# Kernel optimization log

Hardware: AMD Instinct MI355X
Metric: run time of the kernel (lower is better)

## Reference

```python
import jax, jax.numpy as jnp
import numpy as np
from jax import lax

EPS = 1e-5

def _bn(x):
    # BatchNorm1d, training-mode batch stats, affine at init (gamma=1, beta=0)
    return (x - x.mean(0)) / jnp.sqrt(x.var(0) + EPS)

def _nonlinear(x, W1, W2):
    h = jax.nn.relu(_bn(x @ W1.T))
    return jax.nn.relu(_bn(h @ W2.T))

def _conv_bn_lrelu(x, w):
    # x: [E, C, L], w: [O, C, 3], padding=1; BN over (batch, length)
    y = lax.conv_general_dilated(x, w, (1,), [(1, 1)], dimension_numbers=('NCH', 'OIH', 'NCH'))
    m = y.mean((0, 2), keepdims=True)
    v = y.var((0, 2), keepdims=True)
    y = (y - m) / jnp.sqrt(v + EPS)
    return jnp.where(y >= 0, y, 0.01 * y)  # LeakyReLU(negative_slope=0.01)

def _curve_encoder(x, c1, c2, c3, fc):
    y = _conv_bn_lrelu(x, c1)
    y = _conv_bn_lrelu(y, c2)
    y = _conv_bn_lrelu(y, c3)
    y = y.mean(-1)            # AdaptiveAvgPool1d(1)
    return _bn(y @ fc.T)      # _fc: Linear(bias=False) + BN, no activation

def _forward(attn_bias, angle, centroid_distance, edge_data, edge_type,
             edge_length, edge_convexity, node_feat,
             sd_emb, virt, angle_W1, angle_W2, cent_W1, cent_W2,
             etype_W1, etype_W2, elen_W1, elen_W2, econv_W1, econv_W2,
             curv_c1, curv_c2, curv_c3, curv_fc, edis_w,
             ec_Wp, ec_W1, ec_W2,
             shortest_distance, edge_path, edge_padding_mask, src, dst):
    B, N, _ = shortest_distance.shape
    H = sd_emb.shape[1]
    D = edge_path.shape[-1]           # multi_hop_max_dist
    n_edge = edge_padding_mask.shape[1]

    bias = jnp.broadcast_to(attn_bias[:, None], (B, H, N + 1, N + 1))

    # shortest-distance / angle / centroid biases, all [B, H, N, N]
    sdb = sd_emb[shortest_distance].transpose(0, 3, 1, 2)
    ang = _nonlinear(angle.reshape(-1, 1), angle_W1, angle_W2).reshape(B, N, N, H).transpose(0, 3, 1, 2)
    cen = _nonlinear(centroid_distance.reshape(-1, 1), cent_W1, cent_W2).reshape(B, N, N, H).transpose(0, 3, 1, 2)

    # --- multi_hop branch ---
    ef = (_curve_encoder(edge_data.transpose(0, 2, 1), curv_c1, curv_c2, curv_c3, curv_fc)
          + _nonlinear(edge_type, etype_W1, etype_W2)
          + _nonlinear(edge_length[:, None], elen_W1, elen_W2)
          + _nonlinear(edge_convexity, econv_W1, econv_W2))     # [E, H]
    # EdgeConv (UV-Net style node_cat): proj(n[src]) + proj(n[dst]) + efeat -> MLP -> BN -> ReLU
    proj = node_feat @ ec_Wp.T
    agg = proj[src] + proj[dst] + ef
    h = jax.nn.relu(_bn(agg @ ec_W1.T)) @ ec_W2.T
    ef2 = jax.nn.relu(_bn(h))                                   # [E, H]

    # edge_padding_mask is all-False, so edge_feature[edge_pos] = ef2 is a plain
    # row-major reshape; slot n_edge stays zero (padding target of edge_path)
    edge_feature = jnp.zeros((B, n_edge + 1, H), dtype=edge_data.dtype)
    edge_feature = edge_feature.at[:, :n_edge].set(ef2.reshape(B, n_edge, H))

    sd_ = jnp.where(shortest_distance == 0, 1, shortest_distance)
    sd_ = jnp.where(sd_ > 1, sd_ - 1, sd_)
    sd_ = jnp.clip(sd_, 0, D)

    ep = edge_path.reshape(B, N * N * D)
    eb = jnp.take_along_axis(edge_feature, ep[:, :, None], axis=1).reshape(B, N, N, D, H)
    Wd = edis_w.reshape(-1, H, H)[:D]                           # [D, H, H]
    eb = jnp.einsum('bijdh,dhk->bijk', eb, Wd)                  # per-hop bmm fused with hop-sum
    eb = eb / (sd_.astype(eb.dtype)[..., None] + 1e-6)
    eb = jnp.nan_to_num(eb)
    ebias = eb.transpose(0, 3, 1, 2)                            # [B, H, N, N]

    bias = bias.at[:, :, 1:, 1:].add(sdb + ang + cen + ebias)
    t = virt.reshape(1, H, 1)
    bias = bias.at[:, :, 1:, 0].add(t)
    bias = bias.at[:, :, 0, :].add(t)
    return bias + attn_bias[:, None]


def setup_inputs() -> dict:
    key = jax.random.key(0)
    ks = iter(jax.random.split(key, 48))
    B, N, H, D = 4, 256, 16, 5
    n_edge, n_pts = 1024, 20
    dim_node, num_distance, num_edge_dis = 256, 512, 128
    E = B * n_edge
    tot_nodes = B * N
    rn = lambda *s: jax.random.normal(next(ks), s, jnp.float32)
    return {
        'attn_bias': rn(B, N + 1, N + 1),
        'shortest_distance': jax.random.randint(next(ks), (B, N, N), 0, num_distance),
        'angle': rn(B, N, N),
        'centroid_distance': rn(B, N, N),
        'edge_path': jax.random.randint(next(ks), (B, N, N, D), 0, n_edge + 1),
        'edge_data': rn(E, n_pts, 12),
        'edge_type': rn(E, 11),
        'edge_length': rn(E),
        'edge_convexity': rn(E, 3),
        'edge_padding_mask': jnp.zeros((B, n_edge), dtype=bool),
        'src': jax.random.randint(next(ks), (E,), 0, tot_nodes),
        'dst': jax.random.randint(next(ks), (E,), 0, tot_nodes),
        'node_feat': rn(tot_nodes, dim_node),
        'sd_emb': (rn(num_distance, H) * 0.02).at[0].set(0.0),  # padding_idx=0
        'virt': rn(1, H) * 0.02,
        'angle_W1': rn(H, 1) * 0.1, 'angle_W2': rn(H, H) * 0.1,
        'cent_W1': rn(H, 1) * 0.1, 'cent_W2': rn(H, H) * 0.1,
        'etype_W1': rn(H, 11) * 0.1, 'etype_W2': rn(H, H) * 0.1,
        'elen_W1': rn(H, 1) * 0.1, 'elen_W2': rn(H, H) * 0.1,
        'econv_W1': rn(H, 3) * 0.1, 'econv_W2': rn(H, H) * 0.1,
        'curv_c1': rn(64, 12, 3) * 0.1, 'curv_c2': rn(128, 64, 3) * 0.05,
        'curv_c3': rn(256, 128, 3) * 0.05, 'curv_fc': rn(H, 256) * 0.05,
        'edis_w': rn(num_edge_dis * H * H, 1) * 0.02,
        'ec_Wp': rn(H, dim_node) * 0.02, 'ec_W1': rn(64, H) * 0.02, 'ec_W2': rn(H, 64) * 0.02,
    }


def reference(attn_bias, shortest_distance, angle, centroid_distance, edge_path,
              edge_data, edge_type, edge_length, edge_convexity, edge_padding_mask,
              src, dst, node_feat, sd_emb, virt, angle_W1, angle_W2, cent_W1, cent_W2,
              etype_W1, etype_W2, elen_W1, elen_W2, econv_W1, econv_W2,
              curv_c1, curv_c2, curv_c3, curv_fc, edis_w, ec_Wp, ec_W1, ec_W2):
    return _forward(attn_bias, angle, centroid_distance, edge_data, edge_type,
                    edge_length, edge_convexity, node_feat,
                    sd_emb, virt, angle_W1, angle_W2, cent_W1, cent_W2,
                    etype_W1, etype_W2, elen_W1, elen_W2, econv_W1, econv_W2,
                    curv_c1, curv_c2, curv_c3, curv_fc, edis_w,
                    ec_Wp, ec_W1, ec_W2,
                    shortest_distance, edge_path, edge_padding_mask, src, dst)
```

## Files before the change

### kernel.cpp

```cpp
#include <hip/hip_runtime.h>

#define EPSB 1e-5f
#define B_ 4
#define N_ 256
#define H_ 16
#define D_ 5
#define E_ 4096
#define M_PAIR (B_*N_*N_)

typedef __attribute__((ext_vector_type(8))) short short8;
typedef __attribute__((ext_vector_type(4))) float f32x4;

enum {
  SO_ANGX = 0,
  SO_CENX = 2,
  SO_MOMA = 16,
  SO_MOMC = 24,
  SO_C1   = 96,  SO_C1Q   = 160,
  SO_C2   = 224, SO_C2Q   = 352,
  SO_C3   = 480, SO_C3Q   = 736,
  SO_FC   = 992, SO_FCQ   = 1008,
  SO_ET1  = 1024, SO_ET1Q = 1040,
  SO_ET2  = 1056, SO_ET2Q = 1072,
  SO_EL1  = 1088, SO_EL1Q = 1104,
  SO_EL2  = 1120, SO_EL2Q = 1136,
  SO_EV1  = 1152, SO_EV1Q = 1168,
  SO_EV2  = 1184, SO_EV2Q = 1200,
  SO_G1   = 1216, SO_G1Q  = 1280,
  SO_G2   = 1344, SO_G2Q  = 1360,
  STATS_FLOATS = 2048
};

static constexpr size_t F_Y13  = 2048;
static constexpr size_t F_Y2   = F_Y13 + 10485760;
static constexpr size_t F_POOL = F_Y2 + 5242880;
static constexpr size_t F_FCB  = F_POOL + 1048576;
static constexpr size_t F_EF   = F_FCB + 65536;
static constexpr size_t F_PROJ = F_EF + 65536;
static constexpr size_t F_Z1EC = F_PROJ + 16384;
static constexpr size_t F_Z2T  = F_Z1EC + 262144;
static constexpr size_t F_G    = F_Z2T + 196608;
static constexpr size_t F_WT2  = F_G + 328000;
static constexpr size_t F_WT3  = F_WT2 + 12288;

__device__ __forceinline__ float waveSum(float v){
  #pragma unroll
  for(int o=32;o;o>>=1) v += __shfl_down(v,o);
  return v;
}

__device__ __forceinline__ ushort f2bf(float f){
  uint u = __float_as_uint(f);
  uint r = (u + 0x7FFF + ((u>>16)&1)) >> 16;
  return (ushort)r;
}
__device__ __forceinline__ float bf2f(ushort u){
  return __uint_as_float(((uint)u)<<16);
}

__device__ __forceinline__ void red32_atomic(float* ws, int so, int soq, float* s, float* q){
  __shared__ float red[4][32];
  int tid=threadIdx.x, lane=tid&63, wid=tid>>6;
  #pragma unroll
  for(int k=0;k<16;k++){
    float rs=waveSum(s[k]), rq=waveSum(q[k]);
    if(lane==0){ red[wid][k]=rs; red[wid][16+k]=rq; }
  }
  __syncthreads();
  if(tid<32){
    float t=red[0][tid]+red[1][tid]+red[2][tid]+red[3][tid];
    atomicAdd(&ws[tid<16 ? so+tid : soq+(tid-16)], t);
  }
}

__global__ __launch_bounds__(256) void k_conv1(const float* __restrict__ ed,
    const float* __restrict__ w, float* __restrict__ ws){
  __shared__ float wsh[64*37];
  __shared__ float xs[8*12*20];
  __shared__ float reds[256], redq[256];
  int tid=threadIdx.x;
  for(int i=tid;i<2304;i+=256){ int o=i/36, r=i%36; wsh[o*37+r]=w[i]; }
  int e0=blockIdx.x*8;
  for(int i=tid;i<1920;i+=256){
    int e=i/240, r=i%240, l=r/12, c=r%12;
    xs[(e*12+c)*20+l]=ed[(size_t)(e0+e)*240+r];
  }
  __syncthreads();
  int o=tid&63, eg=tid>>6;
  ushort* y1=(ushort*)(ws+F_Y13);
  float ssum=0, ssq=0;
  for(int ee=0;ee<2;ee++){
    int e=eg*2+ee;
    float acc[20];
    #pragma unroll
    for(int l=0;l<20;l++) acc[l]=0;
    for(int c=0;c<12;c++){
      float w0=wsh[o*37+c*3], w1=wsh[o*37+c*3+1], w2=wsh[o*37+c*3+2];
      const float* xr=xs+(e*12+c)*20;
      #pragma unroll
      for(int l=0;l<20;l++){
        acc[l]=fmaf(w1,xr[l],acc[l]);
        if(l>0)  acc[l]=fmaf(w0,xr[l-1],acc[l]);
        if(l<19) acc[l]=fmaf(w2,xr[l+1],acc[l]);
      }
    }
    size_t base=((size_t)(e0+e)*20)*64;
    #pragma unroll
    for(int l=0;l<20;l++){
      y1[base+(size_t)l*64+o]=f2bf(acc[l]);
      ssum+=acc[l]; ssq+=acc[l]*acc[l];
    }
  }
  reds[eg*64+o]=ssum; redq[eg*64+o]=ssq;
  __syncthreads();
  if(tid<64){
    atomicAdd(&ws[SO_C1+tid], reds[tid]+reds[64+tid]+reds[128+tid]+reds[192+tid]);
  } else if(tid<128){
    int oo=tid-64;
    atomicAdd(&ws[SO_C1Q+oo], redq[oo]+redq[64+oo]+redq[128+oo]+redq[192+oo]);
  }
}


__device__ void dev_wprep(int bid, const float* __restrict__ c2w,
    const float* __restrict__ c3w, ushort* __restrict__ wt2, ushort* __restrict__ wt3){
  int t = bid*256 + threadIdx.x;
  if(t < 128*192){
    int idx=t;
    int j=idx&7, lane=(idx>>3)&63, ks=(idx>>9)%6, ct=idx/3072;
    int l16=lane&15, lhi=lane>>4;
    int o=ct*16+l16, tap=ks/2, c=(ks%2)*32+lhi*8+j;
    wt2[idx]=f2bf(c2w[(o*64+c)*3+tap]);
  } else {
    int idx=t-128*192;
    if(idx<256*384){
      int j=idx&7, lane=(idx>>3)&63, ks=(idx>>9)%12, ct=idx/6144;
      int l16=lane&15, lhi=lane>>4;
      int o=ct*16+l16, tap=ks/4, c=(ks%4)*32+lhi*8+j;
      wt3[idx]=f2bf(c3w[(o*128+c)*3+tap]);
    }
  }
}

__device__ void dev_proj(int bid, const float* __restrict__ nf,
    const float* __restrict__ Wp, float* __restrict__ ws, char* pool){
  float* wps=(float*)pool;
  int tid=threadIdx.x;
  for(int i=tid;i<4096;i+=256){ wps[(i>>8)*260+(i&255)]=Wp[i]; }
  __syncthreads();
  int t=bid*256+tid;
  int v=t>>4, h=t&15;
  const float4* row=(const float4*)(nf+(size_t)v*256);
  const float4* wr=(const float4*)(wps+h*260);
  float z=0;
  #pragma unroll 8
  for(int c=0;c<64;c++){
    float4 a=row[c], b=wr[c];
    z+=a.x*b.x+a.y*b.y+a.z*b.z+a.w*b.w;
  }
  ws[F_PROJ+t]=z;
}

__device__ void dev_scalar(int bid, const float* __restrict__ ang,
    const float* __restrict__ cen, float* __restrict__ st){
  int tid = bid*256 + threadIdx.x;
  float sa=0, qa=0, sc=0, qc=0;
  for(int i=tid; i<M_PAIR; i += 256*256){
    float a=ang[i], c=cen[i];
    sa+=a; qa+=a*a; sc+=c; qc+=c*c;
  }
  __shared__ float red[4][4];
  int lane=threadIdx.x&63, wid=threadIdx.x>>6;
  sa=waveSum(sa); qa=waveSum(qa); sc=waveSum(sc); qc=waveSum(qc);
  if(lane==0){ red[wid][0]=sa; red[wid][1]=qa; red[wid][2]=sc; red[wid][3]=qc; }
  __syncthreads();
  if(threadIdx.x<4){
    float t=red[0][threadIdx.x]+red[1][threadIdx.x]+red[2][threadIdx.x]+red[3][threadIdx.x];
    atomicAdd(&st[threadIdx.x], t);
  }
}

template<int DIM>
__device__ void dev_sml1(const float* __restrict__ x,
    const float* __restrict__ W1, float* __restrict__ ws, int so, int soq, int bid){
  __shared__ float w1s[176];
  int tid=threadIdx.x;
  if(tid<16*DIM) w1s[tid]=W1[tid];
  __syncthreads();
  int e=bid*256+tid;
  float xv[DIM];
  #pragma unroll
  for(int j=0;j<DIM;j++) xv[j]=x[(size_t)e*DIM+j];
  float s[16], q[16];
  #pragma unroll
  for(int k=0;k<16;k++){
    float z=0;
    #pragma unroll
    for(int j=0;j<DIM;j++) z+=w1s[k*DIM+j]*xv[j];
    s[k]=z; q[k]=z*z;
  }
  red32_atomic(ws, so, soq, s, q);
}

__global__ __launch_bounds__(256) void k_misc(
    const float* __restrict__ c2w, const float* __restrict__ c3w,
    const float* __restrict__ nf, const float* __restrict__ Wp,
    const float* __restrict__ ang, const float* __restrict__ cen,
    const float* __restrict__ et, const float* __restrict__ el, const float* __restrict__ ev,
    const float* __restrict__ etW1, const float* __restrict__ elW1, const float* __restrict__ evW1,
    float* __restrict__ ws){
  __shared__ char pool[16640];
  int bx=blockIdx.x;
  if(bx<480)       dev_wprep(bx, c2w, c3w, (ushort*)(ws+F_WT2), (ushort*)(ws+F_WT3));
  else if(bx<544)  dev_proj(bx-480, nf, Wp, ws, pool);
  else if(bx<800)  dev_scalar(bx-544, ang, cen, ws);
  else {
    int bid=bx-800;
    int g=bid>>4, b2=bid&15;
    if(g==0)      dev_sml1<11>(et,etW1,ws,SO_ET1,SO_ET1Q,b2);
    else if(g==1) dev_sml1<1> (el,elW1,ws,SO_EL1,SO_EL1Q,b2);
    else          dev_sml1<3> (ev,evW1,ws,SO_EV1,SO_EV1Q,b2);
  }
}


__device__ void dev_mom2(int bid, const float* __restrict__ x, float* __restrict__ st,
    int soX, int mo){
  int tid=threadIdx.x;
  float mu = st[soX]*(1.0f/262144.0f);
  float P=0,N=0,Pq=0,Nq=0;
  for(int i=bid*256+tid; i<M_PAIR; i+=32*256){
    float dx=x[i]-mu;
    if(dx>0){ P+=dx; Pq+=dx*dx; } else { N+=dx; Nq+=dx*dx; }
  }
  __shared__ float red[4][4];
  int lane=tid&63, wid=tid>>6;
  P=waveSum(P); N=waveSum(N); Pq=waveSum(Pq); Nq=waveSum(Nq);
  if(lane==0){ red[wid][0]=P; red[wid][1]=N; red[wid][2]=Pq; red[wid][3]=Nq; }
  __syncthreads();
  if(tid<4){
    float t=red[0][tid]+red[1][tid]+red[2][tid]+red[3][tid];
    atomicAdd(&st[mo+tid], t);
  }
}

template<int DIM>
__device__ void dev_sml2(const float* __restrict__ x,
    const float* __restrict__ W1, const float* __restrict__ W2,
    float* __restrict__ ws, int so1, int so1q, int so2, int so2q,
    float* __restrict__ z2out, int bid){
  __shared__ float w1s[176];
  __shared__ float w2s[256];
  __shared__ float mi[16][2];
  int tid=threadIdx.x;
  if(tid<16*DIM) w1s[tid]=W1[tid];
  w2s[tid]=W2[tid];
  if(tid<16){
    float m=ws[so1+tid]*(1.0f/4096.0f);
    float v=ws[so1q+tid]*(1.0f/4096.0f)-m*m; if(v<0)v=0;
    mi[tid][0]=m; mi[tid][1]=rsqrtf(v+EPSB);
  }
  __syncthreads();
  int e=bid*256+tid;
  float xv[DIM];
  #pragma unroll
  for(int j=0;j<DIM;j++) xv[j]=x[(size_t)e*DIM+j];
  float h1[16];
  #pragma unroll
  for(int h=0;h<16;h++){
    float z=0;
    #pragma unroll
    for(int j=0;j<DIM;j++) z+=w1s[h*DIM+j]*xv[j];
    z=(z-mi[h][0])*mi[h][1];
    h1[h]=z>0?z:0;
  }
  float s[16], q[16];
  #pragma unroll
  for(int k=0;k<16;k++){
    float z=0;
    #pragma unroll
    for(int h=0;h<16;h++) z+=w2s[k*16+h]*h1[h];
    z2out[(size_t)e*16+k]=z;
    s[k]=z; q[k]=z*z;
  }
  red32_atomic(ws, so2, so2q, s, q);
}

__global__ __launch_bounds__(256) void k_stats2(
    const float* __restrict__ ang, const float* __restrict__ cen,
    const float* __restrict__ et, const float* __restrict__ el, const float* __restrict__ ev,
    const float* __restrict__ etW1, const float* __restrict__ etW2,
    const float* __restrict__ elW1, const float* __restrict__ elW2,
    const float* __restrict__ evW1, const float* __restrict__ evW2,
    float* __restrict__ ws){
  int bx=blockIdx.x;
  if(bx<32)       dev_mom2(bx, ang, ws, SO_ANGX, SO_MOMA);
  else if(bx<64)  dev_mom2(bx-32, cen, ws, SO_CENX, SO_MOMC);
  else {
    int bid=bx-64;
    int g=bid>>4, b2=bid&15;
    if(g==0)      dev_sml2<11>(et,etW1,etW2,ws,SO_ET1,SO_ET1Q,SO_ET2,SO_ET2Q,ws+F_Z2T,b2);
    else if(g==1) dev_sml2<1> (el,elW1,elW2,ws,SO_EL1,SO_EL1Q,SO_EL2,SO_EL2Q,ws+F_Z2T+65536,b2);
    else          dev_sml2<3> (ev,evW1,evW2,ws,SO_EV1,SO_EV1Q,SO_EV2,SO_EV2Q,ws+F_Z2T+131072,b2);
  }
}

template<int CIN, int OUT, int EPB, int NSPLIT>
__global__ __launch_bounds__(256) void k_convmf(
    const ushort* __restrict__ yin, const ushort* __restrict__ wt,
    ushort* __restrict__ yout, float* __restrict__ ws,
    int soIn, int soInQ, int soOut, int soOutQ)
{
  constexpr int K = CIN*3;
  constexpr int KSTEPS = K/32;
  constexpr int M = EPB*20;
  constexpr int ROWT = M/16;
  constexpr int WCOLT = OUT/(64*NSPLIT);
  constexpr int ROWS = EPB*22;
  constexpr int RBp = CIN*2 + 16;
  constexpr int RWp = RBp/4;
  __shared__ char xsb[ROWS*RBp];
  __shared__ float mi[CIN][2];
  int tid = threadIdx.x;
  int bx = blockIdx.x;
  int eblk = bx / NSPLIT, split = bx % NSPLIT;
  int lane = tid&63, wid = tid>>6;
  int l16 = lane&15, lhi = lane>>4;
  int colbase = (split*4 + wid) * (OUT/(4*NSPLIT));

  short8 bF[WCOLT][KSTEPS];
  #pragma unroll
  for(int n=0;n<WCOLT;n++){
    const ushort* wp = wt + ((size_t)(colbase/16 + n)*KSTEPS)*512 + (size_t)lane*8;
    #pragma unroll
    for(int ks=0;ks<KSTEPS;ks++) bF[n][ks]=*(const short8*)(wp + (size_t)ks*512);
  }

  for(int c=tid; c<CIN; c+=256){
    float m=ws[soIn+c]*(1.0f/81920.0f);
    float v=ws[soInQ+c]*(1.0f/81920.0f)-m*m; if(v<0)v=0;
    mi[c][0]=m; mi[c][1]=rsqrtf(v+EPSB);
  }
  uint* xs32 = (uint*)xsb;
  for(int i=tid; i<EPB*2*(CIN/2); i+=256){
    int e=i/(CIN), r=i%(CIN); int lp = (r < CIN/2)? 0:21; int cw = r%(CIN/2);
    xs32[(e*22+lp)*RWp+cw]=0;
  }
  __syncthreads();
  int e0 = eblk*EPB;
  const ushort* src = yin + (size_t)e0*20*CIN;
  for(int i=tid; i<EPB*20*(CIN/8); i+=256){
    int c8 = i%(CIN/8); int rl = i/(CIN/8);
    int c = c8*8;
    short8 v = *(const short8*)(src + (size_t)rl*CIN + c);
    uint pk[4];
    #pragma unroll
    for(int jj=0;jj<4;jj++){
      float f0 = bf2f((ushort)v[jj*2]);
      float f1 = bf2f((ushort)v[jj*2+1]);
      f0=(f0-mi[c+jj*2  ][0])*mi[c+jj*2  ][1]; f0= f0>=0?f0:0.01f*f0;
      f1=(f1-mi[c+jj*2+1][0])*mi[c+jj*2+1][1]; f1= f1>=0?f1:0.01f*f1;
      pk[jj] = (uint)f2bf(f0) | ((uint)f2bf(f1)<<16);
    }
    int e = rl/20, l=rl%20;
    int row = e*22 + l + 1;
    *(uint4*)(xsb + (size_t)row*RBp + c*2) = make_uint4(pk[0],pk[1],pk[2],pk[3]);
  }
  __syncthreads();

  f32x4 acc[ROWT][WCOLT];
  #pragma unroll
  for(int m=0;m<ROWT;m++)
    #pragma unroll
    for(int n=0;n<WCOLT;n++) acc[m][n]=(f32x4){0,0,0,0};
  int rowc[ROWT];
  #pragma unroll
  for(int m=0;m<ROWT;m++){ int r=m*16+l16; rowc[m]=(r/20)*22 + (r%20); }

  short8 aF0[ROWT], aF1[ROWT];

#define LOADA(ksv, A) { \
    int t_=(ksv)/(CIN/32); int c0_=((ksv)%(CIN/32))*32 + lhi*8; \
    _Pragma("unroll") \
    for(int m=0;m<ROWT;m++){ \
      int row_=rowc[m]+t_; \
      A[m]=*(const short8*)(xsb + (size_t)row_*RBp + c0_*2); } }

#define MFMAK(A, ksv) { \
    _Pragma("unroll") \
    for(int m=0;m<ROWT;m++) \
      _Pragma("unroll") \
      for(int n=0;n<WCOLT;n++) \
        acc[m][n]=__builtin_amdgcn_mfma_f32_16x16x32_bf16(A[m],bF[n][ksv],acc[m][n],0,0,0); }

  LOADA(0, aF0);
  #pragma unroll
  for(int kp=0; kp<KSTEPS/2; kp++){
    LOADA(kp*2+1, aF1);
    MFMAK(aF0, kp*2);
    if(kp*2+2<KSTEPS) LOADA(kp*2+2, aF0);
    MFMAK(aF1, kp*2+1);
  }
#undef LOADA
#undef MFMAK

  #pragma unroll
  for(int n=0;n<WCOLT;n++){
    float s=0,q=0;
    #pragma unroll
    for(int m=0;m<ROWT;m++)
      #pragma unroll
      for(int j=0;j<4;j++){ float a=acc[m][n][j]; s+=a; q+=a*a; }
    s += __shfl_xor(s,16); s += __shfl_xor(s,32);
    q += __shfl_xor(q,16); q += __shfl_xor(q,32);
    if(lhi==0){
      int o = colbase+n*16+l16;
      atomicAdd(&ws[soOut+o], s);
      atomicAdd(&ws[soOutQ+o], q);
    }
  }
  ushort* dst = yout + (size_t)eblk*M*OUT;
  #pragma unroll
  for(int m=0;m<ROWT;m++)
    #pragma unroll
    for(int j=0;j<4;j++){
      int R = m*16 + lhi*4 + j;
      #pragma unroll
      for(int n=0;n<WCOLT;n++)
        dst[(size_t)R*OUT + colbase + n*16 + l16] = f2bf(acc[m][n][j]);
    }
}

__global__ __launch_bounds__(256) void k_poolfc(const float* __restrict__ fcw, float* __restrict__ ws){
  __shared__ float ps[16][260];
  __shared__ float red[4][32];
  __shared__ float mo[256][2];
  int tid=threadIdx.x;
  {
    float m=ws[SO_C3+tid]*(1.0f/81920.0f);
    float v=ws[SO_C3Q+tid]*(1.0f/81920.0f)-m*m; if(v<0)v=0;
    mo[tid][0]=m; mo[tid][1]=rsqrtf(v+EPSB);
  }
  __syncthreads();
  int e0=blockIdx.x*16;
  const ushort* y3=(const ushort*)(ws+F_Y13);
  float m=mo[tid][0], inv=mo[tid][1];
  for(int el=0;el<16;el++){
    const ushort* row=y3+((size_t)(e0+el)*20)*256+tid;
    float s=0;
    #pragma unroll
    for(int l=0;l<20;l++){
      float x=(bf2f(row[(size_t)l*256])-m)*inv;
      s += x>=0.f? x : 0.01f*x;
    }
    ps[el][tid]=s*(1.0f/20.0f);
  }
  __syncthreads();
  int e=tid>>4, h=tid&15;
  const float* wr=fcw+(size_t)h*256;
  float z=0;
  for(int c=0;c<256;c++) z+=ps[e][c]*wr[c];
  ws[F_FCB+(size_t)(e0+e)*16+h]=z;
  float s=z, q=z*z;
  #pragma unroll
  for(int o=16;o<64;o<<=1){ s+=__shfl_down(s,o); q+=__shfl_down(q,o); }
  int lane=tid&63, wid=tid>>6;
  if(lane<16){ red[wid][lane]=s; red[wid][16+lane]=q; }
  __syncthreads();
  if(tid<32){
    float v=red[0][tid]+red[1][tid]+red[2][tid]+red[3][tid];
    atomicAdd(&ws[tid<16? SO_FC+tid : SO_FCQ+(tid-16)], v);
  }
}

__device__ __constant__ int EF_BASES[4][2] = {
  {SO_ET2,SO_ET2Q},{SO_EL2,SO_EL2Q},{SO_EV2,SO_EV2Q},{SO_FC,SO_FCQ}
};

__global__ __launch_bounds__(256) void k_aggef(const int* __restrict__ src, const int* __restrict__ dst,
    const float* __restrict__ ecW1, float* __restrict__ ws){
  __shared__ float w1s[64*17];
  __shared__ float mi[4][16][2];
  __shared__ float aLDS[32][17];
  __shared__ float zLDS[64][33];
  __shared__ float reds[4][64], redq[4][64];
  int tid=threadIdx.x;
  for(int i=tid;i<1024;i+=256) w1s[(i>>4)*17+(i&15)]=ecW1[i];
  if(tid<64){
    int g=tid>>4, h=tid&15;
    float m=ws[EF_BASES[g][0]+h]*(1.0f/4096.0f);
    float v=ws[EF_BASES[g][1]+h]*(1.0f/4096.0f)-m*m; if(v<0)v=0;
    mi[g][h][0]=m; mi[g][h][1]=rsqrtf(v+EPSB);
  }
  __syncthreads();
  int e0=blockIdx.x*32;
  for(int it=tid; it<32*16; it+=256){
    int el=it>>4, h=it&15;
    int e=e0+el;
    float z=ws[F_FCB+(size_t)e*16+h];
    float a=(z-mi[3][h][0])*mi[3][h][1];
    #pragma unroll
    for(int g=0;g<3;g++){
      float z2=ws[F_Z2T+(size_t)g*65536+(size_t)e*16+h];
      float r=(z2-mi[g][h][0])*mi[g][h][1];
      a+= r>0?r:0;
    }
    int s=src[e], d=dst[e];
    a+=ws[F_PROJ+(size_t)s*16+h]+ws[F_PROJ+(size_t)d*16+h];
    aLDS[el][h]=a;
  }
  __syncthreads();
  int o=tid&63, elq=tid>>6;
  float s=0,q=0;
  #pragma unroll
  for(int j=0;j<8;j++){
    int el=elq*8+j;
    float z=0;
    #pragma unroll
    for(int h=0;h<16;h++) z+=w1s[o*17+h]*aLDS[el][h];
    zLDS[o][el]=z;
    s+=z; q+=z*z;
  }
  reds[elq][o]=s; redq[elq][o]=q;
  __syncthreads();
  for(int idx=tid; idx<2048; idx+=256){
    int oo=idx>>5, el=idx&31;
    ws[F_Z1EC+(size_t)oo*E_+e0+el]=zLDS[oo][el];
  }
  if(tid<64){
    atomicAdd(&ws[SO_G1+tid], reds[0][tid]+reds[1][tid]+reds[2][tid]+reds[3][tid]);
  } else if(tid<128){
    int oo=tid-64;
    atomicAdd(&ws[SO_G1Q+oo], redq[0][oo]+redq[1][oo]+redq[2][oo]+redq[3][oo]);
  }
}

__global__ __launch_bounds__(256) void k_ec2(const float* __restrict__ ecW2, float* __restrict__ ws){
  __shared__ float w2s[1024];
  __shared__ float mi[64][2];
  int tid=threadIdx.x;
  for(int i=tid;i<1024;i+=256) w2s[i]=ecW2[i];
  if(tid<64){
    float m=ws[SO_G1+tid]*(1.0f/4096.0f);
    float v=ws[SO_G1Q+tid]*(1.0f/4096.0f)-m*m; if(v<0)v=0;
    mi[tid][0]=m; mi[tid][1]=rsqrtf(v+EPSB);
  }
  __syncthreads();
  int el=tid&63, kq=tid>>6;
  int e=blockIdx.x*64+el;
  float acc[4]={0,0,0,0};
  #pragma unroll 8
  for(int o=0;o<64;o++){
    float z=ws[F_Z1EC+(size_t)o*E_+e];
    float h=(z-mi[o][0])*mi[o][1];
    h=h>0?h:0;
    #pragma unroll
    for(int j=0;j<4;j++) acc[j]+=w2s[(kq*4+j)*64+o]*h;
  }
  #pragma unroll
  for(int j=0;j<4;j++) ws[F_FCB+(size_t)e*16+kq*4+j]=acc[j];
  #pragma unroll
  for(int j=0;j<4;j++){
    float rs=waveSum(acc[j]);
    float rq=waveSum(acc[j]*acc[j]);
    if(el==0){
      atomicAdd(&ws[SO_G2+kq*4+j], rs);
      atomicAdd(&ws[SO_G2Q+kq*4+j], rq);
    }
  }
}

__global__ __launch_bounds__(256) void k_ef2g(const float* __restrict__ edisw, float* __restrict__ ws){
  __shared__ float wd[1280];
  __shared__ float mi[16][2];
  int tid=threadIdx.x;
  for(int i=tid;i<1280;i+=256) wd[i]=edisw[i];
  if(tid<16){
    float m=ws[SO_G2+tid]*(1.0f/4096.0f);
    float va=ws[SO_G2Q+tid]*(1.0f/4096.0f)-m*m; if(va<0)va=0;
    mi[tid][0]=m; mi[tid][1]=rsqrtf(va+EPSB);
  }
  __syncthreads();
  int t=blockIdx.x*256+tid;
  if(t>=4*1025*5) return;
  int bp=t/5, d=t%5;
  int b=bp/1025, pos=bp%1025;
  float ef[16];
  if(pos<1024){
    int e=b*1024+pos;
    #pragma unroll
    for(int k=0;k<16;k++){
      float z=ws[F_FCB+(size_t)e*16+k];
      float v=(z-mi[k][0])*mi[k][1];
      ef[k]= v>0?v:0;
    }
  } else {
    #pragma unroll
    for(int k=0;k<16;k++) ef[k]=0;
  }
  float* g=ws+F_G+(size_t)bp*80+d*16;
  const float* wdd=wd+d*256;
  #pragma unroll
  for(int k=0;k<16;k++){
    float s=0;
    #pragma unroll
    for(int h=0;h<16;h++) s+=ef[h]*wdd[h*16+k];
    g[k]=s;
  }
}

__global__ __launch_bounds__(256) void k_pair(const float* __restrict__ ab,
    const int* __restrict__ sd, const float* __restrict__ ang, const float* __restrict__ cen,
    const int* __restrict__ ep, const float* __restrict__ sdemb,
    const float* __restrict__ angW1, const float* __restrict__ angW2,
    const float* __restrict__ cenW1, const float* __restrict__ cenW2,
    const float* __restrict__ ws, float* __restrict__ out){
  __shared__ float cpa[16],cma[16],m2a[16],i2a[16];
  __shared__ float cpc[16],cmc[16],m2c[16],i2c[16];
  __shared__ float mv[4];
  int tid=threadIdx.x;
  if(tid==0){
    float s=ws[SO_ANGX], q=ws[SO_ANGX+1];
    float mu=s*(1.0f/262144.0f);
    float v=q*(1.0f/262144.0f)-mu*mu; if(v<0)v=0;
    mv[0]=mu; mv[1]=v;
    s=ws[SO_CENX]; q=ws[SO_CENX+1];
    mu=s*(1.0f/262144.0f);
    v=q*(1.0f/262144.0f)-mu*mu; if(v<0)v=0;
    mv[2]=mu; mv[3]=v;
  }
  __syncthreads();
  if(tid<32){
    int k=tid&15; bool isC = tid>=16;
    const float* W1=isC?cenW1:angW1; const float* W2=isC?cenW2:angW2;
    float var=isC?mv[3]:mv[1];
    float cp=0, cm=0;
    for(int h=0;h<16;h++){
      float w=W1[h];
      float A=w*rsqrtf(var*w*w+EPSB);
      float wk=W2[k*16+h];
      if(A>0) cp+=wk*A; else cm+=wk*A;
    }
    int mo = isC? SO_MOMC : SO_MOMA;
    float P=ws[mo], N=ws[mo+1], Pq=ws[mo+2], Nq=ws[mo+3];
    float mean=(cp*P+cm*N)*(1.0f/262144.0f);
    float e2=(cp*cp*Pq+cm*cm*Nq)*(1.0f/262144.0f);
    float v2=e2-mean*mean; if(v2<0)v2=0;
    float iv=rsqrtf(v2+EPSB);
    if(!isC){ cpa[k]=cp; cma[k]=cm; m2a[k]=mean; i2a[k]=iv; }
    else    { cpc[k]=cp; cmc[k]=cm; m2c[k]=mean; i2c[k]=iv; }
  }
  __syncthreads();
  int t=blockIdx.x*256+tid;
  int b=t>>16, rem=t&65535, i=rem>>8, j=rem&255;
  int sdv=sd[t];
  float xa=ang[t], xc0=cen[t];
  float acc[16];
  const float* se=sdemb+(size_t)sdv*16;
  #pragma unroll
  for(int k=0;k<16;k++) acc[k]=se[k];
  {
    float dx=xa-mv[0];
    bool pos=dx>0.f;
    #pragma unroll
    for(int k=0;k<16;k++){
      float z=dx*(pos?cpa[k]:cma[k]);
      float r=(z-m2a[k])*i2a[k];
      acc[k]+= r>0?r:0;
    }
  }
  {
    float dx=xc0-mv[2];
    bool pos=dx>0.f;
    #pragma unroll
    for(int k=0;k<16;k++){
      float z=dx*(pos?cpc[k]:cmc[k]);
      float r=(z-m2c[k])*i2c[k];
      acc[k]+= r>0?r:0;
    }
  }
  {
    int sdm = sdv==0 ? 1 : sdv;
    if(sdm>1) sdm-=1;
    if(sdm>5) sdm=5;
    float inv=1.0f/((float)sdm+1e-6f);
    float eb[16];
    #pragma unroll
    for(int k=0;k<16;k++) eb[k]=0;
    const float* G=ws+F_G;
    #pragma unroll
    for(int d=0;d<5;d++){
      int idx=ep[(size_t)t*5+d];
      const float4* g=(const float4*)(G+(size_t)(b*1025+idx)*80+d*16);
      float4 g0=g[0], g1=g[1], g2=g[2], g3=g[3];
      eb[0]+=g0.x; eb[1]+=g0.y; eb[2]+=g0.z; eb[3]+=g0.w;
      eb[4]+=g1.x; eb[5]+=g1.y; eb[6]+=g1.z; eb[7]+=g1.w;
      eb[8]+=g2.x; eb[9]+=g2.y; eb[10]+=g2.z; eb[11]+=g2.w;
      eb[12]+=g3.x; eb[13]+=g3.y; eb[14]+=g3.z; eb[15]+=g3.w;
    }
    #pragma unroll
    for(int k=0;k<16;k++) acc[k]+=eb[k]*inv;
  }
  float base2=2.0f*ab[(size_t)b*66049+(size_t)(i+1)*257+(j+1)];
  #pragma unroll
  for(int k=0;k<16;k++)
    out[(((size_t)b*16+k)*257+(i+1))*257+(j+1)]=acc[k]+base2;
}

__global__ __launch_bounds__(256) void k_border(const float* __restrict__ ab,
    const float* __restrict__ virt, float* __restrict__ out){
  int t=blockIdx.x*256+threadIdx.x;
  if(t>=4*16*513) return;
  int idx=t%513, bh=t/513;
  int b=bh>>4, h=bh&15;
  float v=virt[h];
  if(idx<257){
    out[(((size_t)b*16+h)*257)*257+idx]=2.0f*ab[(size_t)b*66049+idx]+v;
  } else {
    int p=idx-256;
    out[(((size_t)b*16+h)*257+p)*257]=2.0f*ab[(size_t)b*66049+(size_t)p*257]+v;
  }
}

extern "C" void kernel_launch(void* const* d_in, const int* in_sizes, int n_in,
                              void* d_out, int out_size, void* d_ws, size_t ws_size,
                              hipStream_t stream) {
  const float* ab    =(const float*)d_in[0];
  const int*   sdist =(const int*)  d_in[1];
  const float* ang   =(const float*)d_in[2];
  const float* cen   =(const float*)d_in[3];
  const int*   ep    =(const int*)  d_in[4];
  const float* edata =(const float*)d_in[5];
  const float* etype =(const float*)d_in[6];
  const float* elen  =(const float*)d_in[7];
  const float* econv =(const float*)d_in[8];
  const int*   src   =(const int*)  d_in[10];
  const int*   dst   =(const int*)  d_in[11];
  const float* nf    =(const float*)d_in[12];
  const float* sdemb =(const float*)d_in[13];
  const float* virt  =(const float*)d_in[14];
  const float* angW1 =(const float*)d_in[15];
  const float* angW2 =(const float*)d_in[16];
  const float* cenW1 =(const float*)d_in[17];
  const float* cenW2 =(const float*)d_in[18];
  const float* etW1  =(const float*)d_in[19];
  const float* etW2  =(const float*)d_in[20];
  const float* elW1  =(const float*)d_in[21];
  const float* elW2  =(const float*)d_in[22];
  const float* evW1  =(const float*)d_in[23];
  const float* evW2  =(const float*)d_in[24];
  const float* c1w   =(const float*)d_in[25];
  const float* c2w   =(const float*)d_in[26];
  const float* c3w   =(const float*)d_in[27];
  const float* fcw   =(const float*)d_in[28];
  const float* edisw =(const float*)d_in[29];
  const float* ecWp  =(const float*)d_in[30];
  const float* ecW1  =(const float*)d_in[31];
  const float* ecW2  =(const float*)d_in[32];
  float* ws=(float*)d_ws;
  float* out=(float*)d_out;

  hipMemsetAsync(d_ws, 0, STATS_FLOATS*sizeof(float), stream);

  k_conv1<<<512,256,0,stream>>>(edata,c1w,ws);
  k_misc<<<848,256,0,stream>>>(c2w,c3w,nf,ecWp,ang,cen,
                               etype,elen,econv,etW1,elW1,evW1,ws);
  k_stats2<<<112,256,0,stream>>>(ang,cen,etype,elen,econv,
                                 etW1,etW2,elW1,elW2,evW1,evW2,ws);

  k_convmf<64,128,4,2><<<2048,256,0,stream>>>((const ushort*)(ws+F_Y13),(const ushort*)(ws+F_WT2),
                                              (ushort*)(ws+F_Y2),ws,SO_C1,SO_C1Q,SO_C2,SO_C2Q);
  k_convmf<128,256,4,2><<<2048,256,0,stream>>>((const ushort*)(ws+F_Y2),(const ushort*)(ws+F_WT3),
                                               (ushort*)(ws+F_Y13),ws,SO_C2,SO_C2Q,SO_C3,SO_C3Q);
  k_poolfc<<<256,256,0,stream>>>(fcw,ws);

  k_aggef<<<128,256,0,stream>>>(src,dst,ecW1,ws);
  k_ec2<<<64,256,0,stream>>>(ecW2,ws);
  k_ef2g<<<81,256,0,stream>>>(edisw,ws);

  k_pair<<<1024,256,0,stream>>>(ab,sdist,ang,cen,ep,sdemb,angW1,angW2,cenW1,cenW2,ws,out);
  k_border<<<129,256,0,stream>>>(ab,virt,out);
}
```

Before: 205.3 us.

## Spread conv BN stat atomics over 32 partial slots and XOR-swizzle LDS tile

```diff
diff --git a/kernel.cpp b/kernel.cpp
--- a/kernel.cpp
+++ b/kernel.cpp
@@ -16,9 +16,6 @@
   SO_CENX = 2,
   SO_MOMA = 16,
   SO_MOMC = 24,
-  SO_C1   = 96,  SO_C1Q   = 160,
-  SO_C2   = 224, SO_C2Q   = 352,
-  SO_C3   = 480, SO_C3Q   = 736,
   SO_FC   = 992, SO_FCQ   = 1008,
   SO_ET1  = 1024, SO_ET1Q = 1040,
   SO_ET2  = 1056, SO_ET2Q = 1072,
@@ -28,10 +25,13 @@
   SO_EV2  = 1184, SO_EV2Q = 1200,
   SO_G1   = 1216, SO_G1Q  = 1280,
   SO_G2   = 1344, SO_G2Q  = 1360,
-  STATS_FLOATS = 2048
+  SP_C1   = 2048,
+  SP_C2   = SP_C1 + 32*512,
+  SP_C3   = SP_C2 + 32*512,
+  PSTATS_END = SP_C3 + 32*512
 };
 
-static constexpr size_t F_Y13  = 2048;
+static constexpr size_t F_Y13  = 51200;
 static constexpr size_t F_Y2   = F_Y13 + 10485760;
 static constexpr size_t F_POOL = F_Y2 + 5242880;
 static constexpr size_t F_FCB  = F_POOL + 1048576;
@@ -113,11 +113,12 @@
   }
   reds[eg*64+o]=ssum; redq[eg*64+o]=ssq;
   __syncthreads();
+  int g=blockIdx.x&31;
   if(tid<64){
-    atomicAdd(&ws[SO_C1+tid], reds[tid]+reds[64+tid]+reds[128+tid]+reds[192+tid]);
+    atomicAdd(&ws[SP_C1+g*512+tid], reds[tid]+reds[64+tid]+reds[128+tid]+reds[192+tid]);
   } else if(tid<128){
     int oo=tid-64;
-    atomicAdd(&ws[SO_C1Q+oo], redq[oo]+redq[64+oo]+redq[128+oo]+redq[192+oo]);
+    atomicAdd(&ws[SP_C1+g*512+256+oo], redq[oo]+redq[64+oo]+redq[128+oo]+redq[192+oo]);
   }
 }
 
@@ -309,7 +310,7 @@
 __global__ __launch_bounds__(256) void k_convmf(
     const ushort* __restrict__ yin, const ushort* __restrict__ wt,
     ushort* __restrict__ yout, float* __restrict__ ws,
-    int soIn, int soInQ, int soOut, int soOutQ)
+    int spIn, int spOut)
 {
   constexpr int K = CIN*3;
   constexpr int KSTEPS = K/32;
@@ -317,9 +318,9 @@
   constexpr int ROWT = M/16;
   constexpr int WCOLT = OUT/(64*NSPLIT);
   constexpr int ROWS = EPB*22;
-  constexpr int RBp = CIN*2 + 16;
-  constexpr int RWp = RBp/4;
-  __shared__ char xsb[ROWS*RBp];
+  constexpr int RB = CIN*2;
+  constexpr uint SWZ = RB/16 - 1;
+  __shared__ ushort xs[ROWS*CIN];
   __shared__ float mi[CIN][2];
   int tid = threadIdx.x;
   int bx = blockIdx.x;
@@ -337,14 +338,17 @@
   }
 
   for(int c=tid; c<CIN; c+=256){
-    float m=ws[soIn+c]*(1.0f/81920.0f);
-    float v=ws[soInQ+c]*(1.0f/81920.0f)-m*m; if(v<0)v=0;
+    float s=0,q=0;
+    #pragma unroll
+    for(int g=0;g<32;g++){ s+=ws[spIn+g*512+c]; q+=ws[spIn+g*512+256+c]; }
+    float m=s*(1.0f/81920.0f);
+    float v=q*(1.0f/81920.0f)-m*m; if(v<0)v=0;
     mi[c][0]=m; mi[c][1]=rsqrtf(v+EPSB);
   }
-  uint* xs32 = (uint*)xsb;
+  uint* xs32 = (uint*)xs;
   for(int i=tid; i<EPB*2*(CIN/2); i+=256){
     int e=i/(CIN), r=i%(CIN); int lp = (r < CIN/2)? 0:21; int cw = r%(CIN/2);
-    xs32[(e*22+lp)*RWp+cw]=0;
+    xs32[(e*22+lp)*(CIN/2)+cw]=0;
   }
   __syncthreads();
   int e0 = eblk*EPB;
@@ -364,7 +368,8 @@
     }
     int e = rl/20, l=rl%20;
     int row = e*22 + l + 1;
-    *(uint4*)(xsb + (size_t)row*RBp + c*2) = make_uint4(pk[0],pk[1],pk[2],pk[3]);
+    uint byteoff = (uint)row*RB + (((uint)c*2) ^ (uint)((row&SWZ)<<4));
+    *(uint4*)((char*)xs + byteoff) = make_uint4(pk[0],pk[1],pk[2],pk[3]);
   }
   __syncthreads();
 
@@ -384,7 +389,8 @@
     _Pragma("unroll") \
     for(int m=0;m<ROWT;m++){ \
       int row_=rowc[m]+t_; \
-      A[m]=*(const short8*)(xsb + (size_t)row_*RBp + c0_*2); } }
+      uint off_=(uint)row_*RB + (((uint)c0_*2) ^ (uint)((row_&SWZ)<<4)); \
+      A[m]=*(const short8*)((char*)xs+off_); } }
 
 #define MFMAK(A, ksv) { \
     _Pragma("unroll") \
@@ -404,6 +410,7 @@
 #undef LOADA
 #undef MFMAK
 
+  int g=bx&31;
   #pragma unroll
   for(int n=0;n<WCOLT;n++){
     float s=0,q=0;
@@ -415,8 +422,8 @@
     q += __shfl_xor(q,16); q += __shfl_xor(q,32);
     if(lhi==0){
       int o = colbase+n*16+l16;
-      atomicAdd(&ws[soOut+o], s);
-      atomicAdd(&ws[soOutQ+o], q);
+      atomicAdd(&ws[spOut+g*512+o], s);
+      atomicAdd(&ws[spOut+g*512+256+o], q);
     }
   }
   ushort* dst = yout + (size_t)eblk*M*OUT;
@@ -437,8 +444,11 @@
   __shared__ float mo[256][2];
   int tid=threadIdx.x;
   {
-    float m=ws[SO_C3+tid]*(1.0f/81920.0f);
-    float v=ws[SO_C3Q+tid]*(1.0f/81920.0f)-m*m; if(v<0)v=0;
+    float s=0,q=0;
+    #pragma unroll
+    for(int g=0;g<32;g++){ s+=ws[SP_C3+g*512+tid]; q+=ws[SP_C3+g*512+256+tid]; }
+    float m=s*(1.0f/81920.0f);
+    float v=q*(1.0f/81920.0f)-m*m; if(v<0)v=0;
     mo[tid][0]=m; mo[tid][1]=rsqrtf(v+EPSB);
   }
   __syncthreads();
@@ -760,7 +770,7 @@
   float* ws=(float*)d_ws;
   float* out=(float*)d_out;
 
-  hipMemsetAsync(d_ws, 0, STATS_FLOATS*sizeof(float), stream);
+  hipMemsetAsync(d_ws, 0, PSTATS_END*sizeof(float), stream);
 
   k_conv1<<<512,256,0,stream>>>(edata,c1w,ws);
   k_misc<<<848,256,0,stream>>>(c2w,c3w,nf,ecWp,ang,cen,
@@ -769,9 +779,9 @@
                                  etW1,etW2,elW1,elW2,evW1,evW2,ws);
 
   k_convmf<64,128,4,2><<<2048,256,0,stream>>>((const ushort*)(ws+F_Y13),(const ushort*)(ws+F_WT2),
-                                              (ushort*)(ws+F_Y2),ws,SO_C1,SO_C1Q,SO_C2,SO_C2Q);
+                                              (ushort*)(ws+F_Y2),ws,SP_C1,SP_C2);
   k_convmf<128,256,4,2><<<2048,256,0,stream>>>((const ushort*)(ws+F_Y2),(const ushort*)(ws+F_WT3),
-                                               (ushort*)(ws+F_Y13),ws,SO_C2,SO_C2Q,SO_C3,SO_C3Q);
+                                               (ushort*)(ws+F_Y13),ws,SP_C2,SP_C3);
   k_poolfc<<<256,256,0,stream>>>(fcw,ws);
 
   k_aggef<<<128,256,0,stream>>>(src,dst,ecW1,ws);
```

Measured after the change: 185.8 us. -9.5%, faster.
